# Optimization experiments

Hardware: AMD Instinct MI355X
Metric: run time of the kernel (lower is better)

Reference implementation:

```python
import jax, jax.numpy as jnp
import numpy as np

N, E, DIN, DH, DOUT = 100000, 1600000, 512, 128, 40


def setup_inputs() -> dict:
    key = jax.random.key(0)
    ks = jax.random.split(key, 4)
    x = jax.random.normal(ks[0], (N, DIN), dtype=jnp.float32)
    edge_index = jax.random.randint(ks[1], (2, E), 0, N, dtype=jnp.int32)
    W1 = jax.random.normal(ks[2], (DIN, DH), dtype=jnp.float32) / np.sqrt(DIN).astype(np.float32)
    b1 = jnp.zeros((DH,), jnp.float32)
    W2 = jax.random.normal(ks[3], (DH, DOUT), dtype=jnp.float32) / np.sqrt(DH).astype(np.float32)
    b2 = jnp.zeros((DOUT,), jnp.float32)
    return {"x": x, "edge_index": edge_index, "W1": W1, "b1": b1, "W2": W2, "b2": b2}


def _gcn_conv(x, W, b, src, dst, norm, n):
    # PyG GCNConv: linear transform first, then normalized neighbor aggregation
    h = x @ W                                   # [n, d_out]
    msg = h[src] * norm[:, None]                # gather + scale, [E+n, d_out]
    out = jax.ops.segment_sum(msg, dst, num_segments=n)  # scatter-add
    return out + b


def reference(x, edge_index, W1, b1, W2, b2):
    n = x.shape[0]
    loops = jnp.arange(n, dtype=edge_index.dtype)
    src = jnp.concatenate([edge_index[0], loops])   # with self-loops
    dst = jnp.concatenate([edge_index[1], loops])
    deg = jax.ops.segment_sum(jnp.ones_like(dst, dtype=jnp.float32), dst, num_segments=n)
    dinv = jnp.where(deg > 0, jax.lax.rsqrt(jnp.maximum(deg, 1.0)), 0.0)
    norm = dinv[src] * dinv[dst]                    # deg^{-1/2}[j] * deg^{-1/2}[i]
    h = jax.nn.relu(_gcn_conv(x, W1, b1, src, dst, norm, n))
    # dropout p=0.5 is a no-op in eval mode (training=False)
    h = _gcn_conv(h, W2, b2, src, dst, norm, n)
    return h, jax.nn.log_softmax(h, axis=1)
```

## Files before the change

kernel.cpp:

```cpp
#include <hip/hip_runtime.h>
#include <math.h>


typedef unsigned int uint;
typedef unsigned short ushort_t;
using short8  = __attribute__((ext_vector_type(8))) short;
using float4v = __attribute__((ext_vector_type(4))) float;

__device__ __forceinline__ ushort_t f2bf(float f) {
    uint u = __float_as_uint(f);
    u += 0x7FFFu + ((u >> 16) & 1u);
    return (ushort_t)(u >> 16);
}
__device__ __forceinline__ float2 unpack2(uint v) {
    return make_float2(__uint_as_float(v << 16), __uint_as_float(v & 0xFFFF0000u));
}
__device__ __forceinline__ uint pack2(float a, float b) {
    return (uint)f2bf(a) | ((uint)f2bf(b) << 16);
}
__device__ __forceinline__ void acc8(float* acc, uint4 v) {
    float2 a0 = unpack2(v.x), a1 = unpack2(v.y), a2 = unpack2(v.z), a3 = unpack2(v.w);
    acc[0] += a0.x; acc[1] += a0.y; acc[2] += a1.x; acc[3] += a1.y;
    acc[4] += a2.x; acc[5] += a2.y; acc[6] += a3.x; acc[7] += a3.y;
}
__device__ __forceinline__ void acc8s(float* acc, uint4 v, float d) {
    float2 a0 = unpack2(v.x), a1 = unpack2(v.y), a2 = unpack2(v.z), a3 = unpack2(v.w);
    acc[0] = fmaf(d, a0.x, acc[0]); acc[1] = fmaf(d, a0.y, acc[1]);
    acc[2] = fmaf(d, a1.x, acc[2]); acc[3] = fmaf(d, a1.y, acc[3]);
    acc[4] = fmaf(d, a2.x, acc[4]); acc[5] = fmaf(d, a2.y, acc[5]);
    acc[6] = fmaf(d, a3.x, acc[6]); acc[7] = fmaf(d, a3.y, acc[7]);
}

__device__ __forceinline__ void gemm1_block(int gb, const float* __restrict__ x,
                                            const ushort_t* __restrict__ W1t,
                                            ushort_t* __restrict__ h, int n) {
    __shared__ ushort_t As[64][72];
    __shared__ ushort_t Bs[128][72];
    const int tid  = threadIdx.x;
    const int w    = tid >> 6, lane = tid & 63;
    const int quad = lane >> 4, l16 = lane & 15;
    const int row0 = gb * 64;

    float4v acc[8];
#pragma unroll
    for (int i = 0; i < 8; i++) acc[i] = (float4v)0.f;

    const int ar  = tid >> 2;
    const int akq = (tid & 3) * 16;
    const int br  = tid >> 1;
    const int bkq = (tid & 1) * 32;
    const int agrow = row0 + ar;
    const float* xp0 = &x[(size_t)agrow * 512];
    const ushort_t* wp0 = &W1t[(size_t)br * 512];

    for (int kb = 0; kb < 512; kb += 64) {
#pragma unroll
        for (int j = 0; j < 4; j++) {
            float4 v = make_float4(0.f, 0.f, 0.f, 0.f);
            if (agrow < n) v = *(const float4*)(xp0 + kb + akq + j * 4);
            ushort4 b;
            b.x = f2bf(v.x); b.y = f2bf(v.y); b.z = f2bf(v.z); b.w = f2bf(v.w);
            *(ushort4*)&As[ar][akq + j * 4] = b;
        }
#pragma unroll
        for (int j = 0; j < 8; j++) {
            *(ushort4*)&Bs[br][bkq + j * 4] = *(const ushort4*)(wp0 + kb + bkq + j * 4);
        }
        __syncthreads();
#pragma unroll
        for (int ks = 0; ks < 64; ks += 32) {
            short8 a = *(const short8*)&As[w * 16 + l16][ks + quad * 8];
#pragma unroll
            for (int ct = 0; ct < 8; ct++) {
                short8 b = *(const short8*)&Bs[ct * 16 + l16][ks + quad * 8];
                acc[ct] = __builtin_amdgcn_mfma_f32_16x16x32_bf16(a, b, acc[ct], 0, 0, 0);
            }
        }
        __syncthreads();
    }
#pragma unroll
    for (int r = 0; r < 4; r++) {
        int grow = row0 + w * 16 + quad * 4 + r;
        if (grow >= n) continue;
#pragma unroll
        for (int ct = 0; ct < 8; ct++) {
            int col = ct * 16 + l16;
            h[(size_t)grow * 128 + col] = f2bf(acc[ct][r]);
        }
    }
}

__global__ __launch_bounds__(256) void k_prep(const float* __restrict__ W1,
                                              const float* __restrict__ W2,
                                              ushort_t* __restrict__ W1t,
                                              ushort_t* __restrict__ W2t,
                                              int* __restrict__ bcnt, int nb) {
    int idx = blockIdx.x * 256 + threadIdx.x;
    if (idx < 65536) {
        int nn = idx >> 9, k = idx & 511;
        W1t[idx] = f2bf(W1[(size_t)k * 128 + nn]);
    } else if (idx < 71680) {
        int j = idx - 65536;
        int c = j >> 7, k = j & 127;
        W2t[j] = (c < 40) ? f2bf(W2[(size_t)k * 40 + c]) : (ushort_t)0;
    } else {
        int j = idx - 71680;
        if (j < nb) bcnt[j] = 0;
    }
}

__global__ __launch_bounds__(256) void k_d2(const int* __restrict__ dst,
                                            int* __restrict__ bcnt, int e, int nb, int nblkA,
                                            const float* __restrict__ x,
                                            const ushort_t* __restrict__ W1t,
                                            ushort_t* __restrict__ h, int n, int goff) {
    if ((int)blockIdx.x >= nblkA) {
        gemm1_block((int)blockIdx.x - nblkA + goff, x, W1t, h, n);
        return;
    }
    __shared__ int sh[800];
    for (int t = threadIdx.x; t < nb; t += 256) sh[t] = 0;
    __syncthreads();
    int ibase = blockIdx.x * 2560 + threadIdx.x;
#pragma unroll
    for (int j = 0; j < 10; j++) {
        int i = ibase + j * 256;
        if (i < e) atomicAdd(&sh[dst[i] >> 7], 1);
    }
    __syncthreads();
    for (int t = threadIdx.x; t < nb; t += 256) {
        int c = sh[t];
        if (c) atomicAdd(&bcnt[t], c);
    }
}

__global__ __launch_bounds__(256) void k_d3(const int* __restrict__ bcnt, int* __restrict__ bbase,
                                            int* __restrict__ bcur, int* __restrict__ row_ptr,
                                            int nb, int n, int e,
                                            const float* __restrict__ x,
                                            const ushort_t* __restrict__ W1t,
                                            ushort_t* __restrict__ h, int goff) {
    if (blockIdx.x > 0) {
        gemm1_block((int)blockIdx.x - 1 + goff, x, W1t, h, n);
        return;
    }
    __shared__ int sd[256];
    int t = threadIdx.x;
    int base = t * 4;
    int v[4];
#pragma unroll
    for (int j = 0; j < 4; j++) v[j] = (base + j < nb) ? bcnt[base + j] : 0;
    int s0 = v[0], s1 = s0 + v[1], s2 = s1 + v[2], s3 = s2 + v[3];
    sd[t] = s3;
    __syncthreads();
    for (int d = 1; d < 256; d <<= 1) {
        int xv = (t >= d) ? sd[t - d] : 0;
        __syncthreads();
        sd[t] += xv;
        __syncthreads();
    }
    int excl = sd[t] - s3;
    int pre0 = excl, pre1 = excl + s0, pre2 = excl + s1, pre3 = excl + s2;
    if (base + 0 < nb) { bbase[base + 0] = pre0; bcur[base + 0] = pre0; }
    if (base + 1 < nb) { bbase[base + 1] = pre1; bcur[base + 1] = pre1; }
    if (base + 2 < nb) { bbase[base + 2] = pre2; bcur[base + 2] = pre2; }
    if (base + 3 < nb) { bbase[base + 3] = pre3; bcur[base + 3] = pre3; }
    if (t == 255) bbase[nb] = excl + s3;
    if (t == 0) row_ptr[n] = e;
}

__global__ __launch_bounds__(256) void k_d4(const int* __restrict__ src, const int* __restrict__ dst,
                                            int* __restrict__ bcur, uint* __restrict__ pbuf,
                                            int e, int nb, int nblkA,
                                            const float* __restrict__ x,
                                            const ushort_t* __restrict__ W1t,
                                            ushort_t* __restrict__ h, int n, int goff) {
    if ((int)blockIdx.x >= nblkA) {
        gemm1_block((int)blockIdx.x - nblkA + goff, x, W1t, h, n);
        return;
    }
    __shared__ int sh[800];
    __shared__ int base_l[800];
    for (int t = threadIdx.x; t < nb; t += 256) sh[t] = 0;
    __syncthreads();
    uint pk[10]; int bk[10]; int lp[10];
    int ibase = blockIdx.x * 2560 + threadIdx.x;
#pragma unroll
    for (int j = 0; j < 10; j++) {
        int i = ibase + j * 256;
        bk[j] = -1;
        if (i < e) {
            int s = src[i], d = dst[i];
            int b = d >> 7;
            bk[j] = b;
            pk[j] = ((uint)(d & 127) << 25) | (uint)s;
            lp[j] = atomicAdd(&sh[b], 1);
        }
    }
    __syncthreads();
    for (int t = threadIdx.x; t < nb; t += 256) {
        int c = sh[t];
        base_l[t] = c ? atomicAdd(&bcur[t], c) : 0;
    }
    __syncthreads();
#pragma unroll
    for (int j = 0; j < 10; j++) {
        if (bk[j] >= 0) pbuf[base_l[bk[j]] + lp[j]] = pk[j];
    }
}

__global__ __launch_bounds__(256) void k_d5(const uint* __restrict__ pbuf,
                                            const int* __restrict__ bbase,
                                            float* __restrict__ dinv,
                                            int* __restrict__ row_ptr,
                                            int* __restrict__ es_src, int n, int nb,
                                            const float* __restrict__ x,
                                            const ushort_t* __restrict__ W1t,
                                            ushort_t* __restrict__ h, int goff) {
    if ((int)blockIdx.x >= nb) {
        gemm1_block((int)blockIdx.x - nb + goff, x, W1t, h, n);
        return;
    }
    __shared__ int cl[128];
    __shared__ int cur[128];
    const int b = blockIdx.x;
    const int tid = threadIdx.x;
    const int ebeg = bbase[b], eend = bbase[b + 1];
    const int m = eend - ebeg;
    if (tid < 128) cl[tid] = 0;
    __syncthreads();
    for (int i = tid; i < m; i += 256) {
        uint p = pbuf[ebeg + i];
        atomicAdd(&cl[p >> 25], 1);
    }
    __syncthreads();
    int own = (tid < 128) ? cl[tid] : 0;
    for (int d = 1; d < 128; d <<= 1) {
        int v = 0;
        if (tid < 128 && tid >= d) v = cl[tid - d];
        __syncthreads();
        if (tid < 128 && tid >= d) cl[tid] += v;
        __syncthreads();
    }
    if (tid < 128) {
        int excl = cl[tid] - own;
        int node = b * 128 + tid;
        if (node < n) {
            dinv[node] = rsqrtf((float)(own + 1));
            row_ptr[node] = ebeg + excl;
        }
        cur[tid] = excl;
    }
    __syncthreads();
    for (int i = tid; i < m; i += 256) {
        uint p = pbuf[ebeg + i];
        int dl = (int)(p >> 25);
        int pos = atomicAdd(&cur[dl], 1);
        es_src[ebeg + pos] = (int)(p & 0x1FFFFFFu);
    }
}

__global__ __launch_bounds__(256) void k_agg1(const uint* __restrict__ h,
                                              const int* __restrict__ row_ptr,
                                              const int* __restrict__ es_src,
                                              const float* __restrict__ dinv,
                                              const float* __restrict__ b1,
                                              uint* __restrict__ h1, int n) {
    const int tid  = threadIdx.x;
    const int node = blockIdx.x * 4 + (tid >> 6);
    if (node >= n) return;
    const int lane = tid & 63;
    const int g4   = lane >> 4;
    const int l16  = lane & 15;
    const int k0 = row_ptr[node], k1 = row_ptr[node + 1];
    const float di = dinv[node];

    uint4 sv = *(const uint4*)&h[(size_t)node * 64 + l16 * 4];

    float acc[8];
#pragma unroll
    for (int i = 0; i < 8; i++) acc[i] = 0.f;

    int k = k0 + g4;
    for (; k + 4 < k1; k += 8) {
        int s0 = es_src[k];
        int s1 = es_src[k + 4];
        float d0 = dinv[s0], d1 = dinv[s1];
        uint4 v0 = *(const uint4*)&h[(size_t)s0 * 64 + l16 * 4];
        uint4 v1 = *(const uint4*)&h[(size_t)s1 * 64 + l16 * 4];
        acc8s(acc, v0, d0);
        acc8s(acc, v1, d1);
    }
    for (; k < k1; k += 4) {
        int s0 = es_src[k];
        float d0 = dinv[s0];
        uint4 v0 = *(const uint4*)&h[(size_t)s0 * 64 + l16 * 4];
        acc8s(acc, v0, d0);
    }

#pragma unroll
    for (int i = 0; i < 8; i++) {
        acc[i] += __shfl_xor(acc[i], 16);
        acc[i] += __shfl_xor(acc[i], 32);
    }
    acc8s(acc, sv, di);

    float4 ba = *(const float4*)&b1[l16 * 8];
    float4 bb = *(const float4*)&b1[l16 * 8 + 4];
    float r[8];
    r[0] = di * acc[0] + ba.x; r[1] = di * acc[1] + ba.y;
    r[2] = di * acc[2] + ba.z; r[3] = di * acc[3] + ba.w;
    r[4] = di * acc[4] + bb.x; r[5] = di * acc[5] + bb.y;
    r[6] = di * acc[6] + bb.z; r[7] = di * acc[7] + bb.w;
#pragma unroll
    for (int i = 0; i < 8; i++) r[i] = r[i] > 0.f ? r[i] : 0.f;

    if (g4 == 0) {
        uint4 o;
        o.x = pack2(r[0], r[1]); o.y = pack2(r[2], r[3]);
        o.z = pack2(r[4], r[5]); o.w = pack2(r[6], r[7]);
        *(uint4*)&h1[(size_t)node * 64 + l16 * 4] = o;
    }
}

__global__ __launch_bounds__(256) void k_gemm2(const ushort_t* __restrict__ h1,
                                               const ushort_t* __restrict__ W2t,
                                               const float* __restrict__ dinv,
                                               ushort_t* __restrict__ g, int n) {
    __shared__ ushort_t As[64][136];
    __shared__ ushort_t Bs[48][136];
    const int tid  = threadIdx.x;
    const int w    = tid >> 6, lane = tid & 63;
    const int quad = lane >> 4, l16 = lane & 15;
    const int row0 = blockIdx.x * 64;

    {
        int ar = tid >> 2;
        int ak = (tid & 3) * 32;
        int grow = row0 + ar;
#pragma unroll
        for (int j = 0; j < 4; j++) {
            uint4 v = make_uint4(0, 0, 0, 0);
            if (grow < n) v = *(const uint4*)&h1[(size_t)grow * 128 + ak + j * 8];
            *(uint4*)&As[ar][ak + j * 8] = v;
        }
    }
    for (int i = tid; i < 768; i += 256) {
        int row = i >> 4, q = i & 15;
        *(uint4*)&Bs[row][q * 8] = *(const uint4*)&W2t[(size_t)row * 128 + q * 8];
    }
    __syncthreads();

    float4v acc[3];
#pragma unroll
    for (int i = 0; i < 3; i++) acc[i] = (float4v)0.f;
#pragma unroll
    for (int ks = 0; ks < 128; ks += 32) {
        short8 a = *(const short8*)&As[w * 16 + l16][ks + quad * 8];
#pragma unroll
        for (int ct = 0; ct < 3; ct++) {
            short8 b = *(const short8*)&Bs[ct * 16 + l16][ks + quad * 8];
            acc[ct] = __builtin_amdgcn_mfma_f32_16x16x32_bf16(a, b, acc[ct], 0, 0, 0);
        }
    }
#pragma unroll
    for (int r = 0; r < 4; r++) {
        int grow = row0 + w * 16 + quad * 4 + r;
        if (grow >= n) continue;
        float di = dinv[grow];
#pragma unroll
        for (int ct = 0; ct < 3; ct++) {
            int col = ct * 16 + l16;
            g[(size_t)grow * 64 + col] = f2bf(di * acc[ct][r]);
        }
        g[(size_t)grow * 64 + 48 + l16] = (ushort_t)0;
    }
}

__global__ __launch_bounds__(256) void k_agg2(const uint* __restrict__ g,
                                              const int* __restrict__ row_ptr,
                                              const int* __restrict__ es_src,
                                              const float* __restrict__ dinv,
                                              const float* __restrict__ b2,
                                              float* __restrict__ out1,
                                              float* __restrict__ out2, int n) {
    const int tid  = threadIdx.x;
    const int node = blockIdx.x * 4 + (tid >> 6);
    if (node >= n) return;
    const int lane = tid & 63;
    const int g8   = lane >> 3;
    const int l8   = lane & 7;
    const int k0 = row_ptr[node], k1 = row_ptr[node + 1];

    uint4 sv = *(const uint4*)&g[(size_t)node * 32 + l8 * 4];

    float acc[8];
#pragma unroll
    for (int i = 0; i < 8; i++) acc[i] = 0.f;

    int k = k0 + g8;
    for (; k + 8 < k1; k += 16) {
        int s0 = es_src[k];
        int s1 = es_src[k + 8];
        uint4 v0 = *(const uint4*)&g[(size_t)s0 * 32 + l8 * 4];
        uint4 v1 = *(const uint4*)&g[(size_t)s1 * 32 + l8 * 4];
        acc8(acc, v0);
        acc8(acc, v1);
    }
    for (; k < k1; k += 8) {
        int s0 = es_src[k];
        uint4 v0 = *(const uint4*)&g[(size_t)s0 * 32 + l8 * 4];
        acc8(acc, v0);
    }

#pragma unroll
    for (int i = 0; i < 8; i++) {
        acc[i] += __shfl_xor(acc[i], 8);
        acc[i] += __shfl_xor(acc[i], 16);
        acc[i] += __shfl_xor(acc[i], 32);
    }
    acc8(acc, sv);

    const float di = dinv[node];
    float v[8];
    if (l8 < 5) {
        float4 ba = *(const float4*)&b2[l8 * 8];
        float4 bb = *(const float4*)&b2[l8 * 8 + 4];
        v[0] = di * acc[0] + ba.x; v[1] = di * acc[1] + ba.y;
        v[2] = di * acc[2] + ba.z; v[3] = di * acc[3] + ba.w;
        v[4] = di * acc[4] + bb.x; v[5] = di * acc[5] + bb.y;
        v[6] = di * acc[6] + bb.z; v[7] = di * acc[7] + bb.w;
    } else {
#pragma unroll
        for (int i = 0; i < 8; i++) v[i] = 0.f;
    }

    float m = -1e30f;
    if (l8 < 5) {
#pragma unroll
        for (int i = 0; i < 8; i++) m = fmaxf(m, v[i]);
    }
#pragma unroll
    for (int d = 1; d < 8; d <<= 1) m = fmaxf(m, __shfl_xor(m, d));
    float s = 0.f;
    if (l8 < 5) {
#pragma unroll
        for (int i = 0; i < 8; i++) s += expf(v[i] - m);
    }
#pragma unroll
    for (int d = 1; d < 8; d <<= 1) s += __shfl_xor(s, d);
    float ls = logf(s) + m;

    if (l8 < 5) {
        if (g8 == 0) {
            *(float4*)&out1[(size_t)node * 40 + l8 * 8]     = make_float4(v[0], v[1], v[2], v[3]);
            *(float4*)&out1[(size_t)node * 40 + l8 * 8 + 4] = make_float4(v[4], v[5], v[6], v[7]);
        } else if (g8 == 1) {
            *(float4*)&out2[(size_t)node * 40 + l8 * 8] =
                make_float4(v[0] - ls, v[1] - ls, v[2] - ls, v[3] - ls);
            *(float4*)&out2[(size_t)node * 40 + l8 * 8 + 4] =
                make_float4(v[4] - ls, v[5] - ls, v[6] - ls, v[7] - ls);
        }
    }
}

static inline size_t align4(size_t v) { return (v + 3) & ~(size_t)3; }

extern "C" void kernel_launch(void* const* d_in, const int* in_sizes, int n_in,
                              void* d_out, int out_size, void* d_ws, size_t ws_size,
                              hipStream_t stream) {
    const float* x  = (const float*)d_in[0];
    const int*   ei = (const int*)d_in[1];
    const float* W1 = (const float*)d_in[2];
    const float* b1 = (const float*)d_in[3];
    const float* W2 = (const float*)d_in[4];
    const float* b2 = (const float*)d_in[5];

    const int n = in_sizes[0] / 512;
    const int e = in_sizes[1] / 2;
    const int* src = ei;
    const int* dst = ei + e;
    const int NB = (n + 127) >> 7;

    char* p = (char*)d_ws;
    int*      bcnt    = (int*)p;        p += align4(NB) * 4;
    int*      bbase   = (int*)p;        p += align4(NB + 1) * 4;
    int*      bcur    = (int*)p;        p += align4(NB) * 4;
    int*      row_ptr = (int*)p;        p += align4(n + 1) * 4;
    float*    dinv    = (float*)p;      p += align4(n) * 4;
    uint*     pbuf    = (uint*)p;       p += align4(e) * 4;
    int*      es_src  = (int*)p;        p += align4(e) * 4;
    ushort_t* W1t     = (ushort_t*)p;   p += (size_t)128 * 512 * 2;
    ushort_t* W2t     = (ushort_t*)p;   p += (size_t)48 * 128 * 2;
    ushort_t* h       = (ushort_t*)p;   p += (size_t)n * 128 * 2;
    ushort_t* h1      = (ushort_t*)p;   p += (size_t)n * 128 * 2;
    ushort_t* g       = h;
    float*    out1    = (float*)d_out;
    float*    out2    = out1 + (size_t)n * 40;

    const int B = 256;
    const int nblkA = (e + 2559) / 2560;
    const int NG = (n + 63) / 64;
    const int c  = (NG + 3) / 4;
    const int c3 = NG - 3 * c;

    k_prep<<<(71680 + NB + 255) / 256, B, 0, stream>>>(W1, W2, W1t, W2t, bcnt, NB);

    k_d2<<<nblkA + c, B, 0, stream>>>(dst, bcnt, e, NB, nblkA, x, W1t, h, n, 0);
    k_d3<<<1 + c, B, 0, stream>>>(bcnt, bbase, bcur, row_ptr, NB, n, e, x, W1t, h, c);
    k_d4<<<nblkA + c, B, 0, stream>>>(src, dst, bcur, pbuf, e, NB, nblkA, x, W1t, h, n, 2 * c);
    k_d5<<<NB + c3, B, 0, stream>>>(pbuf, bbase, dinv, row_ptr, es_src, n, NB, x, W1t, h, 3 * c);

    k_agg1<<<(n + 3) / 4, B, 0, stream>>>((const uint*)h, row_ptr, es_src, dinv, b1, (uint*)h1, n);

    k_gemm2<<<(n + 63) / 64, B, 0, stream>>>(h1, W2t, dinv, g, n);
    k_agg2<<<(n + 3) / 4, B, 0, stream>>>((const uint*)g, row_ptr, es_src, dinv, b2, out1, out2, n);
}
```

Baseline: 518.4 us.

## Fuse layer-1 aggregation with second GEMM and merge weight prep into histogram kernel

Layer-1 neighbor aggregation now runs in a single kernel with the second GEMM. Each block aggregates its 64 rows into shared memory and feeds them straight to MFMA, so the h1 intermediate never makes a round trip through global memory. Weight transposition moves into the first histogram kernel, and bcnt is zeroed with a memset. The first GEMM is now spread over three preprocessing kernels instead of four. The cost is that the fused kernel has each wave walk 16 nodes in sequence with 64 threads per node, and launches far fewer blocks, so latency hiding in the gather may suffer.

New measurement: 552.4 us. +6.6%, slower.

```diff
diff --git a/kernel.cpp b/kernel.cpp
--- a/kernel.cpp
+++ b/kernel.cpp
@@ -90,32 +90,22 @@
     }
 }
 
-__global__ __launch_bounds__(256) void k_prep(const float* __restrict__ W1,
-                                              const float* __restrict__ W2,
-                                              ushort_t* __restrict__ W1t,
-                                              ushort_t* __restrict__ W2t,
-                                              int* __restrict__ bcnt, int nb) {
-    int idx = blockIdx.x * 256 + threadIdx.x;
-    if (idx < 65536) {
-        int nn = idx >> 9, k = idx & 511;
-        W1t[idx] = f2bf(W1[(size_t)k * 128 + nn]);
-    } else if (idx < 71680) {
-        int j = idx - 65536;
-        int c = j >> 7, k = j & 127;
-        W2t[j] = (c < 40) ? f2bf(W2[(size_t)k * 40 + c]) : (ushort_t)0;
-    } else {
-        int j = idx - 71680;
-        if (j < nb) bcnt[j] = 0;
-    }
-}
-
-__global__ __launch_bounds__(256) void k_d2(const int* __restrict__ dst,
+__global__ __launch_bounds__(256) void k_d1(const int* __restrict__ dst,
                                             int* __restrict__ bcnt, int e, int nb, int nblkA,
-                                            const float* __restrict__ x,
-                                            const ushort_t* __restrict__ W1t,
-                                            ushort_t* __restrict__ h, int n, int goff) {
+                                            const float* __restrict__ W1,
+                                            const float* __restrict__ W2,
+                                            ushort_t* __restrict__ W1t,
+                                            ushort_t* __restrict__ W2t) {
     if ((int)blockIdx.x >= nblkA) {
-        gemm1_block((int)blockIdx.x - nblkA + goff, x, W1t, h, n);
+        int idx = ((int)blockIdx.x - nblkA) * 256 + threadIdx.x;
+        if (idx < 65536) {
+            int nn = idx >> 9, k = idx & 511;
+            W1t[idx] = f2bf(W1[(size_t)k * 128 + nn]);
+        } else if (idx < 71680) {
+            int j = idx - 65536;
+            int c = j >> 7, k = j & 127;
+            W2t[j] = (c < 40) ? f2bf(W2[(size_t)k * 40 + c]) : (ushort_t)0;
+        }
         return;
     }
     __shared__ int sh[800];
@@ -134,7 +124,7 @@
     }
 }
 
-__global__ __launch_bounds__(256) void k_d3(const int* __restrict__ bcnt, int* __restrict__ bbase,
+__global__ __launch_bounds__(256) void k_d2(const int* __restrict__ bcnt, int* __restrict__ bbase,
                                             int* __restrict__ bcur, int* __restrict__ row_ptr,
                                             int nb, int n, int e,
                                             const float* __restrict__ x,
@@ -169,7 +159,7 @@
     if (t == 0) row_ptr[n] = e;
 }
 
-__global__ __launch_bounds__(256) void k_d4(const int* __restrict__ src, const int* __restrict__ dst,
+__global__ __launch_bounds__(256) void k_d3(const int* __restrict__ src, const int* __restrict__ dst,
                                             int* __restrict__ bcur, uint* __restrict__ pbuf,
                                             int e, int nb, int nblkA,
                                             const float* __restrict__ x,
@@ -209,7 +199,7 @@
     }
 }
 
-__global__ __launch_bounds__(256) void k_d5(const uint* __restrict__ pbuf,
+__global__ __launch_bounds__(256) void k_d4(const uint* __restrict__ pbuf,
                                             const int* __restrict__ bbase,
                                             float* __restrict__ dinv,
                                             int* __restrict__ row_ptr,
@@ -260,97 +250,84 @@
     }
 }
 
-__global__ __launch_bounds__(256) void k_agg1(const uint* __restrict__ h,
-                                              const int* __restrict__ row_ptr,
-                                              const int* __restrict__ es_src,
-                                              const float* __restrict__ dinv,
-                                              const float* __restrict__ b1,
-                                              uint* __restrict__ h1, int n) {
-    const int tid  = threadIdx.x;
-    const int node = blockIdx.x * 4 + (tid >> 6);
-    if (node >= n) return;
-    const int lane = tid & 63;
-    const int g4   = lane >> 4;
-    const int l16  = lane & 15;
-    const int k0 = row_ptr[node], k1 = row_ptr[node + 1];
-    const float di = dinv[node];
-
-    uint4 sv = *(const uint4*)&h[(size_t)node * 64 + l16 * 4];
-
-    float acc[8];
-#pragma unroll
-    for (int i = 0; i < 8; i++) acc[i] = 0.f;
-
-    int k = k0 + g4;
-    for (; k + 4 < k1; k += 8) {
-        int s0 = es_src[k];
-        int s1 = es_src[k + 4];
-        float d0 = dinv[s0], d1 = dinv[s1];
-        uint4 v0 = *(const uint4*)&h[(size_t)s0 * 64 + l16 * 4];
-        uint4 v1 = *(const uint4*)&h[(size_t)s1 * 64 + l16 * 4];
-        acc8s(acc, v0, d0);
-        acc8s(acc, v1, d1);
-    }
-    for (; k < k1; k += 4) {
-        int s0 = es_src[k];
-        float d0 = dinv[s0];
-        uint4 v0 = *(const uint4*)&h[(size_t)s0 * 64 + l16 * 4];
-        acc8s(acc, v0, d0);
-    }
-
-#pragma unroll
-    for (int i = 0; i < 8; i++) {
-        acc[i] += __shfl_xor(acc[i], 16);
-        acc[i] += __shfl_xor(acc[i], 32);
-    }
-    acc8s(acc, sv, di);
-
-    float4 ba = *(const float4*)&b1[l16 * 8];
-    float4 bb = *(const float4*)&b1[l16 * 8 + 4];
-    float r[8];
-    r[0] = di * acc[0] + ba.x; r[1] = di * acc[1] + ba.y;
-    r[2] = di * acc[2] + ba.z; r[3] = di * acc[3] + ba.w;
-    r[4] = di * acc[4] + bb.x; r[5] = di * acc[5] + bb.y;
-    r[6] = di * acc[6] + bb.z; r[7] = di * acc[7] + bb.w;
-#pragma unroll
-    for (int i = 0; i < 8; i++) r[i] = r[i] > 0.f ? r[i] : 0.f;
-
-    if (g4 == 0) {
-        uint4 o;
-        o.x = pack2(r[0], r[1]); o.y = pack2(r[2], r[3]);
-        o.z = pack2(r[4], r[5]); o.w = pack2(r[6], r[7]);
-        *(uint4*)&h1[(size_t)node * 64 + l16 * 4] = o;
-    }
-}
-
-__global__ __launch_bounds__(256) void k_gemm2(const ushort_t* __restrict__ h1,
-                                               const ushort_t* __restrict__ W2t,
-                                               const float* __restrict__ dinv,
-                                               ushort_t* __restrict__ g, int n) {
+__global__ __launch_bounds__(256) void k_aggemm(const uint* __restrict__ h,
+                                                const int* __restrict__ row_ptr,
+                                                const int* __restrict__ es_src,
+                                                const float* __restrict__ dinv,
+                                                const float* __restrict__ b1,
+                                                const ushort_t* __restrict__ W2t,
+                                                ushort_t* __restrict__ g, int n) {
     __shared__ ushort_t As[64][136];
     __shared__ ushort_t Bs[48][136];
     const int tid  = threadIdx.x;
     const int w    = tid >> 6, lane = tid & 63;
-    const int quad = lane >> 4, l16 = lane & 15;
     const int row0 = blockIdx.x * 64;
-
-    {
-        int ar = tid >> 2;
-        int ak = (tid & 3) * 32;
-        int grow = row0 + ar;
-#pragma unroll
-        for (int j = 0; j < 4; j++) {
-            uint4 v = make_uint4(0, 0, 0, 0);
-            if (grow < n) v = *(const uint4*)&h1[(size_t)grow * 128 + ak + j * 8];
-            *(uint4*)&As[ar][ak + j * 8] = v;
-        }
-    }
+    const int g4   = lane >> 4;
+    const int l16  = lane & 15;
+
     for (int i = tid; i < 768; i += 256) {
         int row = i >> 4, q = i & 15;
         *(uint4*)&Bs[row][q * 8] = *(const uint4*)&W2t[(size_t)row * 128 + q * 8];
     }
-    __syncthreads();
-
+
+    for (int i = 0; i < 16; i++) {
+        const int r    = w * 16 + i;
+        const int node = row0 + r;
+        if (node >= n) {
+            if (g4 == 0) *(uint4*)&As[r][l16 * 8] = make_uint4(0, 0, 0, 0);
+            continue;
+        }
+        const int k0 = row_ptr[node], k1 = row_ptr[node + 1];
+        const float di = dinv[node];
+        uint4 sv = *(const uint4*)&h[(size_t)node * 64 + l16 * 4];
+
+        float acc[8];
+#pragma unroll
+        for (int j = 0; j < 8; j++) acc[j] = 0.f;
+
+        int k = k0 + g4;
+        for (; k + 4 < k1; k += 8) {
+            int s0 = es_src[k];
+            int s1 = es_src[k + 4];
+            float d0 = dinv[s0], d1 = dinv[s1];
+            uint4 v0 = *(const uint4*)&h[(size_t)s0 * 64 + l16 * 4];
+            uint4 v1 = *(const uint4*)&h[(size_t)s1 * 64 + l16 * 4];
+            acc8s(acc, v0, d0);
+            acc8s(acc, v1, d1);
+        }
+        for (; k < k1; k += 4) {
+            int s0 = es_src[k];
+            float d0 = dinv[s0];
+            uint4 v0 = *(const uint4*)&h[(size_t)s0 * 64 + l16 * 4];
+            acc8s(acc, v0, d0);
+        }
+#pragma unroll
+        for (int j = 0; j < 8; j++) {
+            acc[j] += __shfl_xor(acc[j], 16);
+            acc[j] += __shfl_xor(acc[j], 32);
+        }
+        acc8s(acc, sv, di);
+
+        float4 ba = *(const float4*)&b1[l16 * 8];
+        float4 bb = *(const float4*)&b1[l16 * 8 + 4];
+        float rr[8];
+        rr[0] = di * acc[0] + ba.x; rr[1] = di * acc[1] + ba.y;
+        rr[2] = di * acc[2] + ba.z; rr[3] = di * acc[3] + ba.w;
+        rr[4] = di * acc[4] + bb.x; rr[5] = di * acc[5] + bb.y;
+        rr[6] = di * acc[6] + bb.z; rr[7] = di * acc[7] + bb.w;
+#pragma unroll
+        for (int j = 0; j < 8; j++) rr[j] = rr[j] > 0.f ? rr[j] : 0.f;
+
+        if (g4 == 0) {
+            uint4 o;
+            o.x = pack2(rr[0], rr[1]); o.y = pack2(rr[2], rr[3]);
+            o.z = pack2(rr[4], rr[5]); o.w = pack2(rr[6], rr[7]);
+            *(uint4*)&As[r][l16 * 8] = o;
+        }
+    }
+    __syncthreads();
+
+    const int quad = lane >> 4;
     float4v acc[3];
 #pragma unroll
     for (int i = 0; i < 3; i++) acc[i] = (float4v)0.f;
@@ -493,26 +470,24 @@
     ushort_t* W1t     = (ushort_t*)p;   p += (size_t)128 * 512 * 2;
     ushort_t* W2t     = (ushort_t*)p;   p += (size_t)48 * 128 * 2;
     ushort_t* h       = (ushort_t*)p;   p += (size_t)n * 128 * 2;
-    ushort_t* h1      = (ushort_t*)p;   p += (size_t)n * 128 * 2;
-    ushort_t* g       = h;
+    ushort_t* g       = (ushort_t*)p;   p += (size_t)n * 64 * 2;
     float*    out1    = (float*)d_out;
     float*    out2    = out1 + (size_t)n * 40;
 
     const int B = 256;
     const int nblkA = (e + 2559) / 2560;
     const int NG = (n + 63) / 64;
-    const int c  = (NG + 3) / 4;
-    const int c3 = NG - 3 * c;
-
-    k_prep<<<(71680 + NB + 255) / 256, B, 0, stream>>>(W1, W2, W1t, W2t, bcnt, NB);
-
-    k_d2<<<nblkA + c, B, 0, stream>>>(dst, bcnt, e, NB, nblkA, x, W1t, h, n, 0);
-    k_d3<<<1 + c, B, 0, stream>>>(bcnt, bbase, bcur, row_ptr, NB, n, e, x, W1t, h, c);
-    k_d4<<<nblkA + c, B, 0, stream>>>(src, dst, bcur, pbuf, e, NB, nblkA, x, W1t, h, n, 2 * c);
-    k_d5<<<NB + c3, B, 0, stream>>>(pbuf, bbase, dinv, row_ptr, es_src, n, NB, x, W1t, h, 3 * c);
-
-    k_agg1<<<(n + 3) / 4, B, 0, stream>>>((const uint*)h, row_ptr, es_src, dinv, b1, (uint*)h1, n);
-
-    k_gemm2<<<(n + 63) / 64, B, 0, stream>>>(h1, W2t, dinv, g, n);
+    const int c  = (NG + 2) / 3;
+    const int c2 = NG - 2 * c;
+
+    hipMemsetAsync(bcnt, 0, (size_t)NB * 4, stream);
+
+    k_d1<<<nblkA + 281, B, 0, stream>>>(dst, bcnt, e, NB, nblkA, W1, W2, W1t, W2t);
+    k_d2<<<1 + c, B, 0, stream>>>(bcnt, bbase, bcur, row_ptr, NB, n, e, x, W1t, h, 0);
+    k_d3<<<nblkA + c, B, 0, stream>>>(src, dst, bcur, pbuf, e, NB, nblkA, x, W1t, h, n, c);
+    k_d4<<<NB + c2, B, 0, stream>>>(pbuf, bbase, dinv, row_ptr, es_src, n, NB, x, W1t, h, 2 * c);
+
+    k_aggemm<<<NG, B, 0, stream>>>((const uint*)h, row_ptr, es_src, dinv, b1, W2t, g, n);
+
     k_agg2<<<(n + 3) / 4, B, 0, stream>>>((const uint*)g, row_ptr, es_src, dinv, b2, out1, out2, n);
 }
```

## Merge weight prep into histogram kernel and batch neighbor index loads via shuffles

Applied to the files above, without the earlier changes.

Weight transposition to bf16 now runs as extra blocks inside the first dst-histogram kernel, bcnt is zeroed with a memset, and the GEMM1 work is spread over three overlapped kernels instead of four. In both aggregation kernels each wavefront now loads up to 32 or 64 neighbor indices (and dinv values) in one coalesced read and broadcasts them with shuffles, replacing per-lane scattered index loads. This cuts dependent index-load latency in the gather loops. The cost is extra shuffle instructions and some idle lanes on low-degree nodes.

Measured after the change: 536.7 us. 1.04x slower.

```diff
diff --git a/kernel.cpp b/kernel.cpp
--- a/kernel.cpp
+++ b/kernel.cpp
@@ -90,32 +90,22 @@
     }
 }
 
-__global__ __launch_bounds__(256) void k_prep(const float* __restrict__ W1,
-                                              const float* __restrict__ W2,
-                                              ushort_t* __restrict__ W1t,
-                                              ushort_t* __restrict__ W2t,
-                                              int* __restrict__ bcnt, int nb) {
-    int idx = blockIdx.x * 256 + threadIdx.x;
-    if (idx < 65536) {
-        int nn = idx >> 9, k = idx & 511;
-        W1t[idx] = f2bf(W1[(size_t)k * 128 + nn]);
-    } else if (idx < 71680) {
-        int j = idx - 65536;
-        int c = j >> 7, k = j & 127;
-        W2t[j] = (c < 40) ? f2bf(W2[(size_t)k * 40 + c]) : (ushort_t)0;
-    } else {
-        int j = idx - 71680;
-        if (j < nb) bcnt[j] = 0;
-    }
-}
-
-__global__ __launch_bounds__(256) void k_d2(const int* __restrict__ dst,
+__global__ __launch_bounds__(256) void k_d1(const int* __restrict__ dst,
                                             int* __restrict__ bcnt, int e, int nb, int nblkA,
-                                            const float* __restrict__ x,
-                                            const ushort_t* __restrict__ W1t,
-                                            ushort_t* __restrict__ h, int n, int goff) {
+                                            const float* __restrict__ W1,
+                                            const float* __restrict__ W2,
+                                            ushort_t* __restrict__ W1t,
+                                            ushort_t* __restrict__ W2t) {
     if ((int)blockIdx.x >= nblkA) {
-        gemm1_block((int)blockIdx.x - nblkA + goff, x, W1t, h, n);
+        int idx = ((int)blockIdx.x - nblkA) * 256 + threadIdx.x;
+        if (idx < 65536) {
+            int nn = idx >> 9, k = idx & 511;
+            W1t[idx] = f2bf(W1[(size_t)k * 128 + nn]);
+        } else if (idx < 71680) {
+            int j = idx - 65536;
+            int c = j >> 7, k = j & 127;
+            W2t[j] = (c < 40) ? f2bf(W2[(size_t)k * 40 + c]) : (ushort_t)0;
+        }
         return;
     }
     __shared__ int sh[800];
@@ -134,7 +124,7 @@
     }
 }
 
-__global__ __launch_bounds__(256) void k_d3(const int* __restrict__ bcnt, int* __restrict__ bbase,
+__global__ __launch_bounds__(256) void k_d2(const int* __restrict__ bcnt, int* __restrict__ bbase,
                                             int* __restrict__ bcur, int* __restrict__ row_ptr,
                                             int nb, int n, int e,
                                             const float* __restrict__ x,
@@ -169,7 +159,7 @@
     if (t == 0) row_ptr[n] = e;
 }
 
-__global__ __launch_bounds__(256) void k_d4(const int* __restrict__ src, const int* __restrict__ dst,
+__global__ __launch_bounds__(256) void k_d3(const int* __restrict__ src, const int* __restrict__ dst,
                                             int* __restrict__ bcur, uint* __restrict__ pbuf,
                                             int e, int nb, int nblkA,
                                             const float* __restrict__ x,
@@ -209,7 +199,7 @@
     }
 }
 
-__global__ __launch_bounds__(256) void k_d5(const uint* __restrict__ pbuf,
+__global__ __launch_bounds__(256) void k_d4(const uint* __restrict__ pbuf,
                                             const int* __restrict__ bbase,
                                             float* __restrict__ dinv,
                                             int* __restrict__ row_ptr,
@@ -281,21 +271,26 @@
 #pragma unroll
     for (int i = 0; i < 8; i++) acc[i] = 0.f;
 
-    int k = k0 + g4;
-    for (; k + 4 < k1; k += 8) {
-        int s0 = es_src[k];
-        int s1 = es_src[k + 4];
-        float d0 = dinv[s0], d1 = dinv[s1];
-        uint4 v0 = *(const uint4*)&h[(size_t)s0 * 64 + l16 * 4];
-        uint4 v1 = *(const uint4*)&h[(size_t)s1 * 64 + l16 * 4];
-        acc8s(acc, v0, d0);
-        acc8s(acc, v1, d1);
-    }
-    for (; k < k1; k += 4) {
-        int s0 = es_src[k];
-        float d0 = dinv[s0];
-        uint4 v0 = *(const uint4*)&h[(size_t)s0 * 64 + l16 * 4];
-        acc8s(acc, v0, d0);
+    int k = k0;
+    while (k < k1) {
+        int rem = k1 - k;
+        int cnt = rem < 32 ? rem : 32;
+        int idx = 0; float dv = 0.f;
+        if (lane < cnt) {
+            idx = es_src[k + lane];
+            dv  = dinv[idx];
+        }
+#pragma unroll
+        for (int t = 0; t < 8; t++) {
+            int j = g4 + 4 * t;
+            int   s = __shfl(idx, j);
+            float d = __shfl(dv, j);
+            if (j < cnt) {
+                uint4 v = *(const uint4*)&h[(size_t)s * 64 + l16 * 4];
+                acc8s(acc, v, d);
+            }
+        }
+        k += cnt;
     }
 
 #pragma unroll
@@ -398,19 +393,22 @@
 #pragma unroll
     for (int i = 0; i < 8; i++) acc[i] = 0.f;
 
-    int k = k0 + g8;
-    for (; k + 8 < k1; k += 16) {
-        int s0 = es_src[k];
-        int s1 = es_src[k + 8];
-        uint4 v0 = *(const uint4*)&g[(size_t)s0 * 32 + l8 * 4];
-        uint4 v1 = *(const uint4*)&g[(size_t)s1 * 32 + l8 * 4];
-        acc8(acc, v0);
-        acc8(acc, v1);
-    }
-    for (; k < k1; k += 8) {
-        int s0 = es_src[k];
-        uint4 v0 = *(const uint4*)&g[(size_t)s0 * 32 + l8 * 4];
-        acc8(acc, v0);
+    int k = k0;
+    while (k < k1) {
+        int rem = k1 - k;
+        int cnt = rem < 64 ? rem : 64;
+        int idx = 0;
+        if (lane < cnt) idx = es_src[k + lane];
+#pragma unroll
+        for (int t = 0; t < 8; t++) {
+            int j = g8 + 8 * t;
+            int s = __shfl(idx, j);
+            if (j < cnt) {
+                uint4 v = *(const uint4*)&g[(size_t)s * 32 + l8 * 4];
+                acc8(acc, v);
+            }
+        }
+        k += cnt;
     }
 
 #pragma unroll
@@ -501,15 +499,15 @@
     const int B = 256;
     const int nblkA = (e + 2559) / 2560;
     const int NG = (n + 63) / 64;
-    const int c  = (NG + 3) / 4;
-    const int c3 = NG - 3 * c;
-
-    k_prep<<<(71680 + NB + 255) / 256, B, 0, stream>>>(W1, W2, W1t, W2t, bcnt, NB);
-
-    k_d2<<<nblkA + c, B, 0, stream>>>(dst, bcnt, e, NB, nblkA, x, W1t, h, n, 0);
-    k_d3<<<1 + c, B, 0, stream>>>(bcnt, bbase, bcur, row_ptr, NB, n, e, x, W1t, h, c);
-    k_d4<<<nblkA + c, B, 0, stream>>>(src, dst, bcur, pbuf, e, NB, nblkA, x, W1t, h, n, 2 * c);
-    k_d5<<<NB + c3, B, 0, stream>>>(pbuf, bbase, dinv, row_ptr, es_src, n, NB, x, W1t, h, 3 * c);
+    const int c  = (NG + 2) / 3;
+    const int c2 = NG - 2 * c;
+
+    hipMemsetAsync(bcnt, 0, (size_t)NB * 4, stream);
+
+    k_d1<<<nblkA + 280, B, 0, stream>>>(dst, bcnt, e, NB, nblkA, W1, W2, W1t, W2t);
+    k_d2<<<1 + c, B, 0, stream>>>(bcnt, bbase, bcur, row_ptr, NB, n, e, x, W1t, h, 0);
+    k_d3<<<nblkA + c, B, 0, stream>>>(src, dst, bcur, pbuf, e, NB, nblkA, x, W1t, h, n, c);
+    k_d4<<<NB + c2, B, 0, stream>>>(pbuf, bbase, dinv, row_ptr, es_src, n, NB, x, W1t, h, 2 * c);
 
     k_agg1<<<(n + 3) / 4, B, 0, stream>>>((const uint*)h, row_ptr, es_src, dinv, b1, (uint*)h1, n);
 
```

## Fold weight prep into histogram kernel and split agg1 rows across two waves

Applied to the files above, without the earlier changes.

Weight transposition/bf16 conversion moves into the first edge-histogram kernel as extra blocks, the bucket-count zeroing becomes a memset, and the GEMM1 blocks are redistributed over three CSR-build kernels instead of four. This drops one kernel launch and the serial prep step before the pipeline. The first-layer aggregation now uses two waves per node, each handling half the 128 feature columns with 8 edges in flight per wave, to raise memory-level parallelism on gathers. In exchange it adds an extra shuffle reduction step and doubles the block count for agg1.

After: 538.6 us. 1.04x slower.

```diff
diff --git a/kernel.cpp b/kernel.cpp
--- a/kernel.cpp
+++ b/kernel.cpp
@@ -90,32 +90,22 @@
     }
 }
 
-__global__ __launch_bounds__(256) void k_prep(const float* __restrict__ W1,
-                                              const float* __restrict__ W2,
-                                              ushort_t* __restrict__ W1t,
-                                              ushort_t* __restrict__ W2t,
-                                              int* __restrict__ bcnt, int nb) {
-    int idx = blockIdx.x * 256 + threadIdx.x;
-    if (idx < 65536) {
-        int nn = idx >> 9, k = idx & 511;
-        W1t[idx] = f2bf(W1[(size_t)k * 128 + nn]);
-    } else if (idx < 71680) {
-        int j = idx - 65536;
-        int c = j >> 7, k = j & 127;
-        W2t[j] = (c < 40) ? f2bf(W2[(size_t)k * 40 + c]) : (ushort_t)0;
-    } else {
-        int j = idx - 71680;
-        if (j < nb) bcnt[j] = 0;
-    }
-}
-
-__global__ __launch_bounds__(256) void k_d2(const int* __restrict__ dst,
+__global__ __launch_bounds__(256) void k_d1(const int* __restrict__ dst,
                                             int* __restrict__ bcnt, int e, int nb, int nblkA,
-                                            const float* __restrict__ x,
-                                            const ushort_t* __restrict__ W1t,
-                                            ushort_t* __restrict__ h, int n, int goff) {
+                                            const float* __restrict__ W1,
+                                            const float* __restrict__ W2,
+                                            ushort_t* __restrict__ W1t,
+                                            ushort_t* __restrict__ W2t) {
     if ((int)blockIdx.x >= nblkA) {
-        gemm1_block((int)blockIdx.x - nblkA + goff, x, W1t, h, n);
+        int idx = ((int)blockIdx.x - nblkA) * 256 + threadIdx.x;
+        if (idx < 65536) {
+            int nn = idx >> 9, k = idx & 511;
+            W1t[idx] = f2bf(W1[(size_t)k * 128 + nn]);
+        } else if (idx < 71680) {
+            int j = idx - 65536;
+            int c = j >> 7, k = j & 127;
+            W2t[j] = (c < 40) ? f2bf(W2[(size_t)k * 40 + c]) : (ushort_t)0;
+        }
         return;
     }
     __shared__ int sh[800];
@@ -134,7 +124,7 @@
     }
 }
 
-__global__ __launch_bounds__(256) void k_d3(const int* __restrict__ bcnt, int* __restrict__ bbase,
+__global__ __launch_bounds__(256) void k_d2(const int* __restrict__ bcnt, int* __restrict__ bbase,
                                             int* __restrict__ bcur, int* __restrict__ row_ptr,
                                             int nb, int n, int e,
                                             const float* __restrict__ x,
@@ -169,7 +159,7 @@
     if (t == 0) row_ptr[n] = e;
 }
 
-__global__ __launch_bounds__(256) void k_d4(const int* __restrict__ src, const int* __restrict__ dst,
+__global__ __launch_bounds__(256) void k_d3(const int* __restrict__ src, const int* __restrict__ dst,
                                             int* __restrict__ bcur, uint* __restrict__ pbuf,
                                             int e, int nb, int nblkA,
                                             const float* __restrict__ x,
@@ -209,7 +199,7 @@
     }
 }
 
-__global__ __launch_bounds__(256) void k_d5(const uint* __restrict__ pbuf,
+__global__ __launch_bounds__(256) void k_d4(const uint* __restrict__ pbuf,
                                             const int* __restrict__ bbase,
                                             float* __restrict__ dinv,
                                             int* __restrict__ row_ptr,
@@ -267,46 +257,51 @@
                                               const float* __restrict__ b1,
                                               uint* __restrict__ h1, int n) {
     const int tid  = threadIdx.x;
-    const int node = blockIdx.x * 4 + (tid >> 6);
+    const int w    = tid >> 6;
+    const int node = blockIdx.x * 2 + (w >> 1);
     if (node >= n) return;
+    const int half = w & 1;
     const int lane = tid & 63;
-    const int g4   = lane >> 4;
-    const int l16  = lane & 15;
+    const int g8   = lane >> 3;
+    const int l8   = lane & 7;
     const int k0 = row_ptr[node], k1 = row_ptr[node + 1];
     const float di = dinv[node];
-
-    uint4 sv = *(const uint4*)&h[(size_t)node * 64 + l16 * 4];
+    const uint ubase = half * 32 + l8 * 4;
+
+    uint4 sv = *(const uint4*)&h[(size_t)node * 64 + ubase];
 
     float acc[8];
 #pragma unroll
     for (int i = 0; i < 8; i++) acc[i] = 0.f;
 
-    int k = k0 + g4;
-    for (; k + 4 < k1; k += 8) {
+    int k = k0 + g8;
+    for (; k + 8 < k1; k += 16) {
         int s0 = es_src[k];
-        int s1 = es_src[k + 4];
+        int s1 = es_src[k + 8];
         float d0 = dinv[s0], d1 = dinv[s1];
-        uint4 v0 = *(const uint4*)&h[(size_t)s0 * 64 + l16 * 4];
-        uint4 v1 = *(const uint4*)&h[(size_t)s1 * 64 + l16 * 4];
+        uint4 v0 = *(const uint4*)&h[(size_t)s0 * 64 + ubase];
+        uint4 v1 = *(const uint4*)&h[(size_t)s1 * 64 + ubase];
         acc8s(acc, v0, d0);
         acc8s(acc, v1, d1);
     }
-    for (; k < k1; k += 4) {
+    for (; k < k1; k += 8) {
         int s0 = es_src[k];
         float d0 = dinv[s0];
-        uint4 v0 = *(const uint4*)&h[(size_t)s0 * 64 + l16 * 4];
+        uint4 v0 = *(const uint4*)&h[(size_t)s0 * 64 + ubase];
         acc8s(acc, v0, d0);
     }
 
 #pragma unroll
     for (int i = 0; i < 8; i++) {
+        acc[i] += __shfl_xor(acc[i], 8);
         acc[i] += __shfl_xor(acc[i], 16);
         acc[i] += __shfl_xor(acc[i], 32);
     }
     acc8s(acc, sv, di);
 
-    float4 ba = *(const float4*)&b1[l16 * 8];
-    float4 bb = *(const float4*)&b1[l16 * 8 + 4];
+    const int cbase = half * 64 + l8 * 8;
+    float4 ba = *(const float4*)&b1[cbase];
+    float4 bb = *(const float4*)&b1[cbase + 4];
     float r[8];
     r[0] = di * acc[0] + ba.x; r[1] = di * acc[1] + ba.y;
     r[2] = di * acc[2] + ba.z; r[3] = di * acc[3] + ba.w;
@@ -315,11 +310,11 @@
 #pragma unroll
     for (int i = 0; i < 8; i++) r[i] = r[i] > 0.f ? r[i] : 0.f;
 
-    if (g4 == 0) {
+    if (g8 == 0) {
         uint4 o;
         o.x = pack2(r[0], r[1]); o.y = pack2(r[2], r[3]);
         o.z = pack2(r[4], r[5]); o.w = pack2(r[6], r[7]);
-        *(uint4*)&h1[(size_t)node * 64 + l16 * 4] = o;
+        *(uint4*)&h1[(size_t)node * 64 + ubase] = o;
     }
 }
 
@@ -501,17 +496,17 @@
     const int B = 256;
     const int nblkA = (e + 2559) / 2560;
     const int NG = (n + 63) / 64;
-    const int c  = (NG + 3) / 4;
-    const int c3 = NG - 3 * c;
-
-    k_prep<<<(71680 + NB + 255) / 256, B, 0, stream>>>(W1, W2, W1t, W2t, bcnt, NB);
-
-    k_d2<<<nblkA + c, B, 0, stream>>>(dst, bcnt, e, NB, nblkA, x, W1t, h, n, 0);
-    k_d3<<<1 + c, B, 0, stream>>>(bcnt, bbase, bcur, row_ptr, NB, n, e, x, W1t, h, c);
-    k_d4<<<nblkA + c, B, 0, stream>>>(src, dst, bcur, pbuf, e, NB, nblkA, x, W1t, h, n, 2 * c);
-    k_d5<<<NB + c3, B, 0, stream>>>(pbuf, bbase, dinv, row_ptr, es_src, n, NB, x, W1t, h, 3 * c);
-
-    k_agg1<<<(n + 3) / 4, B, 0, stream>>>((const uint*)h, row_ptr, es_src, dinv, b1, (uint*)h1, n);
+    const int c  = (NG + 2) / 3;
+    const int c2 = NG - 2 * c;
+
+    hipMemsetAsync(bcnt, 0, (size_t)NB * 4, stream);
+
+    k_d1<<<nblkA + 280, B, 0, stream>>>(dst, bcnt, e, NB, nblkA, W1, W2, W1t, W2t);
+    k_d2<<<1 + c, B, 0, stream>>>(bcnt, bbase, bcur, row_ptr, NB, n, e, x, W1t, h, 0);
+    k_d3<<<nblkA + c, B, 0, stream>>>(src, dst, bcur, pbuf, e, NB, nblkA, x, W1t, h, n, c);
+    k_d4<<<NB + c2, B, 0, stream>>>(pbuf, bbase, dinv, row_ptr, es_src, n, NB, x, W1t, h, 2 * c);
+
+    k_agg1<<<(n + 1) / 2, B, 0, stream>>>((const uint*)h, row_ptr, es_src, dinv, b1, (uint*)h1, n);
 
     k_gemm2<<<(n + 63) / 64, B, 0, stream>>>(h1, W2t, dinv, g, n);
     k_agg2<<<(n + 3) / 4, B, 0, stream>>>((const uint*)g, row_ptr, es_src, dinv, b2, out1, out2, n);
```
